# Kernel optimization log

Hardware: AMD Instinct MI355X
Metric: run time of the kernel (lower is better)

Reference implementation:

```python
import jax, jax.numpy as jnp
import numpy as np

HIDDEN = 2048
N_HEADS = 16
HEAD_DIM = 128
N_KV_HEADS = 4
MAX_POS = 4096
NEG_INF = -1e9


def _fixed_pos_embedding(features, length):
    # matches generate_fixed_pos_embedding: freqs over arange(0, features, 2)/features
    fraction = jnp.arange(0, features, 2, dtype=jnp.float32) / features
    timescale = 10000.0 ** fraction
    inv_freq = 1.0 / timescale
    sinusoid = jnp.einsum('i,j->ij', jnp.arange(length, dtype=jnp.float32), inv_freq)
    sinusoid = jnp.concatenate([sinusoid, sinusoid], axis=-1)  # [length, features]
    return jnp.sin(sinusoid), jnp.cos(sinusoid)


def setup_inputs() -> dict:
    key = jax.random.key(0)
    k0, k1, k2, k3, k4 = jax.random.split(key, 5)
    B, S = 2, 2048
    hidden_states = jax.random.normal(k0, (B, S, HIDDEN), dtype=jnp.float32)
    # causal additive mask [B,1,S,S]; module forces mask[:, :, :, 0] = 0
    causal = jnp.where(jnp.tril(jnp.ones((S, S), dtype=bool)), 0.0, NEG_INF).astype(jnp.float32)
    causal = causal.at[:, 0].set(0.0)
    attention_mask = jnp.broadcast_to(causal[None, None], (B, 1, S, S))
    std = 0.02
    q_w = jax.random.normal(k1, (N_HEADS * HEAD_DIM, HIDDEN), dtype=jnp.float32) * std
    k_w = jax.random.normal(k2, (N_KV_HEADS * HEAD_DIM, HIDDEN), dtype=jnp.float32) * std
    v_w = jax.random.normal(k3, (N_KV_HEADS * HEAD_DIM, HIDDEN), dtype=jnp.float32) * std
    o_w = jax.random.normal(k4, (HIDDEN, N_HEADS * HEAD_DIM), dtype=jnp.float32) * std
    sin, cos = _fixed_pos_embedding(HEAD_DIM, MAX_POS)
    return {"hidden_states": hidden_states, "attention_mask": attention_mask,
            "q_w": q_w, "k_w": k_w, "v_w": v_w, "o_w": o_w, "sin": sin, "cos": cos}


def _rotate_half(x):
    d = x.shape[-1] // 2
    return jnp.concatenate([-x[..., d:], x[..., :d]], axis=-1)


def reference(hidden_states, attention_mask, q_w, k_w, v_w, o_w, sin, cos):
    B, S, _ = hidden_states.shape
    D = cos.shape[-1]
    H = q_w.shape[0] // D
    KV = k_w.shape[0] // D
    n_rep = H // KV

    # QKV projections (nn.Linear: y = x @ W^T), split into heads: [B,S,h,D]
    q = jnp.einsum('bsh,oh->bso', hidden_states, q_w).reshape(B, S, H, D)
    k = jnp.einsum('bsh,oh->bso', hidden_states, k_w).reshape(B, S, KV, D)
    v = jnp.einsum('bsh,oh->bso', hidden_states, v_w).reshape(B, S, KV, D)

    # rotary embedding (non-decode path: q and k share cos/sin[:S])
    c = cos[:S][None, :, None, :]
    s = sin[:S][None, :, None, :]
    q = q * c + _rotate_half(q) * s
    k = k * c + _rotate_half(k) * s

    # repeat_kv (repeat_interleave along head dim) for GQA
    k = jnp.repeat(k, n_rep, axis=2)  # [B,S,H,D]
    v = jnp.repeat(v, n_rep, axis=2)

    # NOTE: no 1/sqrt(D) scaling -- module uses softmax_scale=1.0
    scores = jnp.einsum('bqhd,bkhd->bhqk', q, k) + attention_mask
    weights = jax.nn.softmax(scores.astype(jnp.float32), axis=-1).astype(q.dtype)
    attn = jnp.einsum('bhqk,bkhd->bqhd', weights, v).reshape(B, S, H * D)
    return jnp.einsum('bso,ho->bsh', attn, o_w)
```

## Files before the change

kernel.cpp:

```cpp
#include <hip/hip_runtime.h>

typedef __bf16 bf16x8 __attribute__((ext_vector_type(8)));
typedef float f32x4 __attribute__((ext_vector_type(4)));
typedef float f32x16 __attribute__((ext_vector_type(16)));

#define LOG2E 1.44269504088896340736f

#define GLDS16(g, l) __builtin_amdgcn_global_load_lds(                         \
    (const __attribute__((address_space(1))) unsigned int*)(g),                \
    (__attribute__((address_space(3))) unsigned int*)(l), 16, 0, 0)


__global__ __launch_bounds__(256) void megasplit(
    const float* __restrict__ hs, const float* __restrict__ qw,
    const float* __restrict__ kw, const float* __restrict__ vw,
    const float* __restrict__ ow,
    __bf16* __restrict__ hsh, __bf16* __restrict__ hsl,
    __bf16* __restrict__ wqh, __bf16* __restrict__ wql,
    __bf16* __restrict__ owh, __bf16* __restrict__ owl)
{
    int bid = blockIdx.x;
    const float* src; __bf16* dh; __bf16* dl;
    if (bid < 4096)      { src = hs; dh = hsh; dl = hsl; }
    else if (bid < 6144) { bid -= 4096; src = qw; dh = wqh; dl = wql; }
    else if (bid < 6656) { bid -= 6144; src = kw;
                           dh = wqh + (size_t)2048 * 2048;
                           dl = wql + (size_t)2048 * 2048; }
    else if (bid < 7168) { bid -= 6656; src = vw;
                           dh = wqh + (size_t)2560 * 2048;
                           dl = wql + (size_t)2560 * 2048; }
    else                 { bid -= 7168; src = ow; dh = owh; dl = owl; }

    const size_t t = (size_t)(bid * 256 + threadIdx.x) * 8;
    float4 a = *(const float4*)(src + t);
    float4 b = *(const float4*)(src + t + 4);
    float f[8] = {a.x, a.y, a.z, a.w, b.x, b.y, b.z, b.w};
    bf16x8 h, l;
#pragma unroll
    for (int i = 0; i < 8; ++i) {
        __bf16 hh = (__bf16)f[i];
        h[i] = hh; l[i] = (__bf16)(f[i] - (float)hh);
    }
    const int r  = (int)(t >> 11);
    const int sw = (r ^ (r >> 2)) & 3;
    const size_t d = (t & ~(size_t)31) + ((size_t)((((int)(t >> 3) & 3) ^ sw)) << 3);
    *(bf16x8*)(dh + d) = h;
    *(bf16x8*)(dl + d) = l;
}

template<int BN, int NLOAD>
__global__ __launch_bounds__(512, 2) void gemm_planes32(
    const __bf16* __restrict__ Ah, const __bf16* __restrict__ Al,
    const __bf16* __restrict__ Bh, const __bf16* __restrict__ Bl,
    float* __restrict__ C, int ldc)
{
    constexpr int WN = BN / 2;
    constexpr int CF = WN / 32;
    constexpr int RF = 2;

    __shared__ __bf16 sAh[2][256 * 32];
    __shared__ __bf16 sAl[2][256 * 32];
    __shared__ __bf16 sBh[2][BN * 32];
    __shared__ __bf16 sBl[2][BN * 32];

    const int tid  = threadIdx.x;
    const int lane = tid & 63;
    const int wave = tid >> 6;
    const int wmr  = (wave & 3) * 64;
    const int wnc  = (wave >> 2) * WN;

    const int idg = blockIdx.y * 16 + blockIdx.x;
    const int swb = (idg & 7) * 32 + (idg >> 3);
    const int m0  = (swb >> 4) * 256;
    const int n0  = (swb & 15) * BN;

    const int rl  = lane & 31;
    const int kh  = lane >> 5;
    const int srl = (rl ^ (rl >> 2)) & 3;

    const int srow = tid >> 2;
    const int spb  = (tid & 3) << 3;
    const __bf16* gAh0 = Ah + (size_t)(m0 + srow) * 2048 + spb;
    const __bf16* gAh1 = gAh0 + (size_t)128 * 2048;
    const __bf16* gAl0 = Al + (size_t)(m0 + srow) * 2048 + spb;
    const __bf16* gAl1 = gAl0 + (size_t)128 * 2048;
    const __bf16* gBh0 = Bh + (size_t)(n0 + srow) * 2048 + spb;
    const __bf16* gBl0 = Bl + (size_t)(n0 + srow) * 2048 + spb;
    const __bf16* gX5  = Bl;
    const __bf16* gBl6 = Bl;
    if constexpr (BN == 192) {
        gX5 = (tid < 256)
            ? Bh + (size_t)(n0 + 128 + srow) * 2048 + spb
            : Bl + (size_t)(n0 + ((tid - 256) >> 2)) * 2048 + (((tid - 256) & 3) << 3);
        gBl6 = Bl + (size_t)(n0 + 64 + srow) * 2048 + spb;
    }

#define STAGE8(bb)                                                             \
    do {                                                                       \
        GLDS16(gAh0, &sAh[bb][tid * 8]);                                       \
        GLDS16(gAh1, &sAh[bb][4096 + tid * 8]);                                \
        GLDS16(gAl0, &sAl[bb][tid * 8]);                                       \
        GLDS16(gAl1, &sAl[bb][4096 + tid * 8]);                                \
        GLDS16(gBh0, &sBh[bb][tid * 8]);                                       \
        if constexpr (BN == 192) {                                             \
            if (tid < 256) { GLDS16(gX5, &sBh[bb][4096 + tid * 8]); }          \
            else           { GLDS16(gX5, &sBl[bb][(tid - 256) * 8]); }         \
            GLDS16(gBl6, &sBl[bb][2048 + tid * 8]);                            \
        } else {                                                               \
            GLDS16(gBl0, &sBl[bb][tid * 8]);                                   \
        }                                                                      \
    } while (0)

#define ADV8()                                                                 \
    do {                                                                       \
        gAh0 += 32; gAh1 += 32; gAl0 += 32; gAl1 += 32;                        \
        gBh0 += 32; gBl0 += 32;                                                \
        if constexpr (BN == 192) { gX5 += 32; gBl6 += 32; }                    \
    } while (0)

    f32x16 acc[RF][CF];
#pragma unroll
    for (int rf = 0; rf < RF; ++rf)
#pragma unroll
        for (int cf = 0; cf < CF; ++cf)
            acc[rf][cf] = (f32x16){0.f};

    STAGE8(0);
    ADV8();

    for (int t = 0; t < 64; ++t) {
        const int buf = t & 1;

        __builtin_amdgcn_sched_barrier(0);
        asm volatile("s_waitcnt vmcnt(0)" ::: "memory");
        __builtin_amdgcn_sched_barrier(0);
        __builtin_amdgcn_s_barrier();
        __builtin_amdgcn_sched_barrier(0);
        if (t < 63) {
            STAGE8(buf ^ 1);
            ADV8();
        }
        __builtin_amdgcn_sched_barrier(0);

        __builtin_amdgcn_s_setprio(1);
#pragma unroll
        for (int kk = 0; kk < 2; ++kk) {
            bf16x8 ah[RF], al[RF], bhf[CF], blf[CF];
#pragma unroll
            for (int rf = 0; rf < RF; ++rf) {
                const int ra = (wmr + rf * 32 + rl) * 32
                             + (((kk * 2 + kh) ^ srl) << 3);
                ah[rf] = *(const bf16x8*)&sAh[buf][ra];
                al[rf] = *(const bf16x8*)&sAl[buf][ra];
            }
#pragma unroll
            for (int cf = 0; cf < CF; ++cf) {
                const int rb = (wnc + cf * 32 + rl) * 32
                             + (((kk * 2 + kh) ^ srl) << 3);
                bhf[cf] = *(const bf16x8*)&sBh[buf][rb];
                blf[cf] = *(const bf16x8*)&sBl[buf][rb];
            }
#pragma unroll
            for (int rf = 0; rf < RF; ++rf)
#pragma unroll
                for (int cf = 0; cf < CF; ++cf) {
                    acc[rf][cf] = __builtin_amdgcn_mfma_f32_32x32x16_bf16(
                        ah[rf], bhf[cf], acc[rf][cf], 0, 0, 0);
                    acc[rf][cf] = __builtin_amdgcn_mfma_f32_32x32x16_bf16(
                        al[rf], bhf[cf], acc[rf][cf], 0, 0, 0);
                    acc[rf][cf] = __builtin_amdgcn_mfma_f32_32x32x16_bf16(
                        ah[rf], blf[cf], acc[rf][cf], 0, 0, 0);
                }
        }
        __builtin_amdgcn_s_setprio(0);
    }

#pragma unroll
    for (int rf = 0; rf < RF; ++rf)
#pragma unroll
        for (int cf = 0; cf < CF; ++cf)
#pragma unroll
            for (int reg = 0; reg < 16; ++reg) {
                const int row = m0 + wmr + rf * 32
                              + (reg & 3) + 8 * (reg >> 2) + 4 * kh;
                const int col = n0 + wnc + cf * 32 + rl;
                C[(size_t)row * ldc + col] = acc[rf][cf][reg];
            }
#undef STAGE8
#undef ADV8
}

__global__ __launch_bounds__(256) void rope_prep(
    float* __restrict__ qkv,
    const float* __restrict__ sinp, const float* __restrict__ cosp,
    __bf16* __restrict__ ksp, __bf16* __restrict__ vtsp)
{
    __shared__ float vs[32][132];
    const int tid = threadIdx.x;

    if (blockIdx.x < 16384) {
        int t = blockIdx.x * 256 + tid;
        int row = t >> 10;
        int rem = t & 1023;
        int col = (rem >> 6) * 128 + (rem & 63);
        int s = row & 2047;
        int d = col & 127;

        float* p = qkv + (size_t)row * 3072 + col;
        float x0  = p[0];
        float x1  = p[64];
        float c0  = cosp[s * 128 + d];
        float c1  = cosp[s * 128 + d + 64];
        float sn0 = sinp[s * 128 + d];
        float sn1 = sinp[s * 128 + d + 64];
        p[0]  = x0 * c0 - x1 * sn0;
        p[64] = x1 * c1 + x0 * sn1;
        return;
    }

    const int pidx = blockIdx.x - 16384;
    const int kb  = pidx & 15;
    const int kvh = (pidx >> 4) & 3;
    const int b   = pidx >> 6;

    {
        const int key = tid >> 1;
        const int dh  = (tid & 1) * 32;
        const int pos = kb * 128 + key;
        const int ksw = key & 7;
        const float* src = qkv + (size_t)(b * 2048 + pos) * 3072 + 2048 + kvh * 128;
        __bf16* dst = ksp + ((size_t)((b * 4 + kvh) * 2048) + pos) * 256;
        const float* cp = cosp + pos * 128;
        const float* sp = sinp + pos * 128;
#pragma unroll
        for (int g = 0; g < 4; ++g) {
            int d0 = dh + g * 8;
            float4 x0a = *(const float4*)(src + d0);
            float4 x0b = *(const float4*)(src + d0 + 4);
            float4 x1a = *(const float4*)(src + d0 + 64);
            float4 x1b = *(const float4*)(src + d0 + 68);
            float4 c0a = *(const float4*)(cp + d0);
            float4 c0b = *(const float4*)(cp + d0 + 4);
            float4 c1a = *(const float4*)(cp + d0 + 64);
            float4 c1b = *(const float4*)(cp + d0 + 68);
            float4 s0a = *(const float4*)(sp + d0);
            float4 s0b = *(const float4*)(sp + d0 + 4);
            float4 s1a = *(const float4*)(sp + d0 + 64);
            float4 s1b = *(const float4*)(sp + d0 + 68);
            float x0[8] = {x0a.x,x0a.y,x0a.z,x0a.w,x0b.x,x0b.y,x0b.z,x0b.w};
            float x1[8] = {x1a.x,x1a.y,x1a.z,x1a.w,x1b.x,x1b.y,x1b.z,x1b.w};
            float c0[8] = {c0a.x,c0a.y,c0a.z,c0a.w,c0b.x,c0b.y,c0b.z,c0b.w};
            float c1[8] = {c1a.x,c1a.y,c1a.z,c1a.w,c1b.x,c1b.y,c1b.z,c1b.w};
            float s0[8] = {s0a.x,s0a.y,s0a.z,s0a.w,s0b.x,s0b.y,s0b.z,s0b.w};
            float s1[8] = {s1a.x,s1a.y,s1a.z,s1a.w,s1b.x,s1b.y,s1b.z,s1b.w};
            bf16x8 h0, l0, h1, l1;
#pragma unroll
            for (int i = 0; i < 8; ++i) {
                float y0 = x0[i] * c0[i] - x1[i] * s0[i];
                float y1 = x1[i] * c1[i] + x0[i] * s1[i];
                __bf16 hh0 = (__bf16)y0;
                __bf16 hh1 = (__bf16)y1;
                h0[i] = hh0; l0[i] = (__bf16)(y0 - (float)hh0);
                h1[i] = hh1; l1[i] = (__bf16)(y1 - (float)hh1);
            }
            const int bb = d0 >> 3;
            *(bf16x8*)(dst + ((bb        ^ ksw) << 3)) = h0;
            *(bf16x8*)(dst + (((bb + 8)  ^ ksw) << 3)) = h1;
            *(bf16x8*)(dst + (((bb + 16) ^ ksw) << 3)) = l0;
            *(bf16x8*)(dst + (((bb + 24) ^ ksw) << 3)) = l1;
        }
    }

    for (int st = 0; st < 4; ++st) {
        __syncthreads();
        {
            const int key = tid >> 3;
            const int dc  = (tid & 7) * 16;
            const float* vsrc = qkv + (size_t)(b * 2048 + kb * 128 + st * 32 + key) * 3072
                                + 2560 + kvh * 128 + dc;
            float4 v0 = *(const float4*)(vsrc);
            float4 v1 = *(const float4*)(vsrc + 4);
            float4 v2 = *(const float4*)(vsrc + 8);
            float4 v3 = *(const float4*)(vsrc + 12);
            *(float4*)&vs[key][dc]      = v0;
            *(float4*)&vs[key][dc + 4]  = v1;
            *(float4*)&vs[key][dc + 8]  = v2;
            *(float4*)&vs[key][dc + 12] = v3;
        }
        __syncthreads();
        {
            const int plane = tid >> 7;
            const int d     = tid & 127;
            bf16x8 ob[4];
#pragma unroll
            for (int k = 0; k < 32; ++k) {
                float x = vs[k][d];
                __bf16 hh = (__bf16)x;
                ob[k >> 3][k & 7] = plane ? (__bf16)(x - (float)hh) : hh;
            }
            const int rV  = plane * 128 + d;
            const int vsw = (d >> 1) & 3;
            __bf16* dst = vtsp + ((size_t)((b * 4 + kvh) * 64 + kb * 4 + st)) * 8192
                               + (size_t)rV * 32;
            *(bf16x8*)(dst + ((0 ^ vsw) << 3)) = ob[0];
            *(bf16x8*)(dst + ((1 ^ vsw) << 3)) = ob[1];
            *(bf16x8*)(dst + ((2 ^ vsw) << 3)) = ob[2];
            *(bf16x8*)(dst + ((3 ^ vsw) << 3)) = ob[3];
        }
    }
}

__global__ __launch_bounds__(512, 4) void flash_attn(
    const float* __restrict__ qkv,
    const __bf16* __restrict__ ksp,
    const __bf16* __restrict__ vtsp,
    __bf16* __restrict__ attnh, __bf16* __restrict__ attnl)
{
    __shared__ __bf16 Ks[2][32 * 256];
    __shared__ __bf16 Vt[2][256 * 32];
    __shared__ unsigned int Psf[4][2][512];

    const int tid  = threadIdx.x;
    const int lane = tid & 63;
    const int wave = tid >> 6;
    const int hw   = wave & 3;
    const int rs   = wave >> 2;
    const int id   = blockIdx.x;
    const int pair = id & 7;
    const int kvh  = pair & 3;
    const int b    = pair >> 2;
    const int u    = id >> 3;
    const int qb   = (u >> 5) ? (u & 31) : 63 - (u & 31);
    const int h    = kvh * 4 + hw;

    const int fr  = lane & 15;
    const int g   = lane >> 4;
    const int fc  = g * 8;
    const int dr  = g * 4;
    const int frs = fr & 7;

    bf16x8 aqh[4], aql[4];
    {
        const size_t qrow = (size_t)(b * 2048 + qb * 32 + rs * 16 + fr) * 3072 + h * 128;
#pragma unroll
        for (int ks = 0; ks < 4; ++ks) {
            float4 qv[2];
            qv[0] = *(const float4*)(qkv + qrow + ks * 32 + fc);
            qv[1] = *(const float4*)(qkv + qrow + ks * 32 + fc + 4);
            const float* qf = (const float*)qv;
            bf16x8 h8, l8;
#pragma unroll
            for (int i = 0; i < 8; ++i) {
                float x = qf[i];
                __bf16 hh = (__bf16)x;
                h8[i] = hh; l8[i] = (__bf16)(x - (float)hh);
            }
            aqh[ks] = h8; aql[ks] = l8;
        }
    }
    asm volatile("s_waitcnt vmcnt(0)" ::: "memory");
    __builtin_amdgcn_sched_barrier(0);

    bf16x8 ones;
#pragma unroll
    for (int i = 0; i < 8; ++i) ones[i] = (__bf16)1.0f;

    f32x4 o[8];
#pragma unroll
    for (int dg = 0; dg < 8; ++dg) o[dg] = (f32x4){0.f, 0.f, 0.f, 0.f};
    f32x4 ls = (f32x4){0.f, 0.f, 0.f, 0.f};

    const int ntiles = qb + 1;
    const __bf16* kg0 = ksp + (size_t)(b * 4 + kvh) * 2048 * 256 + wave * 1024 + lane * 8;
    const __bf16* vg0 = vtsp + (size_t)(b * 4 + kvh) * 64 * 8192 + wave * 1024 + lane * 8;

    {
        __bf16* kl = &Ks[0][wave * 1024];
        __bf16* vl = &Vt[0][wave * 1024];
        GLDS16(kg0, kl); GLDS16(kg0 + 512, kl + 512);
        GLDS16(vg0, vl); GLDS16(vg0 + 512, vl + 512);
    }

    for (int kt = 0; kt < ntiles; ++kt) {
        if (kt + 1 < ntiles) {
            const __bf16* kg = kg0 + (size_t)(kt + 1) * 8192;
            const __bf16* vg = vg0 + (size_t)(kt + 1) * 8192;
            __bf16* kl = &Ks[(kt + 1) & 1][wave * 1024];
            __bf16* vl = &Vt[(kt + 1) & 1][wave * 1024];
            GLDS16(kg, kl); GLDS16(kg + 512, kl + 512);
            GLDS16(vg, vl); GLDS16(vg + 512, vl + 512);
            asm volatile("s_waitcnt vmcnt(4)" ::: "memory");
        } else {
            asm volatile("s_waitcnt vmcnt(0)" ::: "memory");
        }
        __builtin_amdgcn_sched_barrier(0);
        __builtin_amdgcn_s_barrier();
        __builtin_amdgcn_sched_barrier(0);

        const int buf = kt & 1;
        const int k0 = kt * 32;

        f32x4 s0v = (f32x4){0.f, 0.f, 0.f, 0.f};
        f32x4 s1v = (f32x4){0.f, 0.f, 0.f, 0.f};
        __builtin_amdgcn_s_setprio(1);
#pragma unroll
        for (int ks = 0; ks < 4; ++ks) {
            const int bh = ks * 4 + g;
            bf16x8 b0h = *(const bf16x8*)&Ks[buf][fr * 256        + ((bh        ^ frs) << 3)];
            bf16x8 b0l = *(const bf16x8*)&Ks[buf][fr * 256        + (((bh + 16) ^ frs) << 3)];
            bf16x8 b1h = *(const bf16x8*)&Ks[buf][(16 + fr) * 256 + ((bh        ^ frs) << 3)];
            bf16x8 b1l = *(const bf16x8*)&Ks[buf][(16 + fr) * 256 + (((bh + 16) ^ frs) << 3)];
            s0v = __builtin_amdgcn_mfma_f32_16x16x32_bf16(aqh[ks], b0h, s0v, 0, 0, 0);
            s0v = __builtin_amdgcn_mfma_f32_16x16x32_bf16(aql[ks], b0h, s0v, 0, 0, 0);
            s0v = __builtin_amdgcn_mfma_f32_16x16x32_bf16(aqh[ks], b0l, s0v, 0, 0, 0);
            s1v = __builtin_amdgcn_mfma_f32_16x16x32_bf16(aqh[ks], b1h, s1v, 0, 0, 0);
            s1v = __builtin_amdgcn_mfma_f32_16x16x32_bf16(aql[ks], b1h, s1v, 0, 0, 0);
            s1v = __builtin_amdgcn_mfma_f32_16x16x32_bf16(aqh[ks], b1l, s1v, 0, 0, 0);
        }
        __builtin_amdgcn_s_setprio(0);

        if (kt == ntiles - 1) {
#pragma unroll
            for (int r = 0; r < 4; ++r) {
                const int qg = qb * 32 + rs * 16 + dr + r;
                if (k0 + fr > qg)      s0v[r] = -1e30f;
                if (k0 + 16 + fr > qg) s1v[r] = -1e30f;
            }
        }
        {
            uint4 w0, w1;
#pragma unroll
            for (int r = 0; r < 4; ++r) {
                float x0 = exp2f(s0v[r] * LOG2E);
                float x1 = exp2f(s1v[r] * LOG2E);
                __bf16 h0 = (__bf16)x0;
                __bf16 h1 = (__bf16)x1;
                unsigned u0 = ((unsigned)__builtin_bit_cast(unsigned short, h0) << 16)
                            |  (unsigned)__builtin_bit_cast(unsigned short, (__bf16)(x0 - (float)h0));
                unsigned u1 = ((unsigned)__builtin_bit_cast(unsigned short, h1) << 16)
                            |  (unsigned)__builtin_bit_cast(unsigned short, (__bf16)(x1 - (float)h1));
                ((unsigned*)&w0)[r] = u0;
                ((unsigned*)&w1)[r] = u1;
            }
            unsigned int* pw = &Psf[hw][rs][0];
            const int sb = (fr * 4 + g) ^ (((fr >> 3) & 1) << 2);
            *(uint4*)(pw + sb * 4)        = w0;
            *(uint4*)(pw + (sb + 64) * 4) = w1;
        }
        asm volatile("s_waitcnt lgkmcnt(0)" ::: "memory");
        __builtin_amdgcn_sched_barrier(0);

        bf16x8 ph, pl;
#pragma unroll
        for (int j = 0; j < 8; ++j) {
            const int col = fc + j;
            const int sR  = (col * 4 + (fr >> 2)) ^ ((g & 1) << 2);
            const unsigned v = Psf[hw][rs][sR * 4 + (fr & 3)];
            ph[j] = __builtin_bit_cast(__bf16, (unsigned short)(v >> 16));
            pl[j] = __builtin_bit_cast(__bf16, (unsigned short)(v & 0xffffu));
        }

        __builtin_amdgcn_s_setprio(1);
        ls = __builtin_amdgcn_mfma_f32_16x16x32_bf16(ph, ones, ls, 0, 0, 0);
        ls = __builtin_amdgcn_mfma_f32_16x16x32_bf16(pl, ones, ls, 0, 0, 0);
#pragma unroll
        for (int dg = 0; dg < 8; ++dg) {
            const int d0 = dg * 16 + fr;
            const int sw = (g ^ ((d0 >> 1) & 3)) << 3;
            bf16x8 bvh = *(const bf16x8*)&Vt[buf][d0 * 32 + sw];
            bf16x8 bvl = *(const bf16x8*)&Vt[buf][(d0 + 128) * 32 + sw];
            o[dg] = __builtin_amdgcn_mfma_f32_16x16x32_bf16(ph, bvh, o[dg], 0, 0, 0);
            o[dg] = __builtin_amdgcn_mfma_f32_16x16x32_bf16(pl, bvh, o[dg], 0, 0, 0);
            o[dg] = __builtin_amdgcn_mfma_f32_16x16x32_bf16(ph, bvl, o[dg], 0, 0, 0);
        }
        __builtin_amdgcn_s_setprio(0);

        __builtin_amdgcn_s_barrier();
    }

    {
        const size_t orow = (size_t)(b * 2048 + qb * 32 + rs * 16);
#pragma unroll
        for (int dg = 0; dg < 8; ++dg)
#pragma unroll
            for (int r = 0; r < 4; ++r) {
                float val = o[dg][r] / ls[r];
                const int rl  = dr + r;
                const int swz = (rl ^ (rl >> 2)) & 3;
                const int col = h * 128 + dg * 16 + fr;
                const size_t idx = (size_t)(orow + rl) * 2048 + (col & ~31)
                                 + ((((col >> 3) & 3) ^ swz) << 3) + (col & 7);
                __bf16 hh = (__bf16)val;
                attnh[idx] = hh;
                attnl[idx] = (__bf16)(val - (float)hh);
            }
    }
}

extern "C" void kernel_launch(void* const* d_in, const int* in_sizes, int n_in,
                              void* d_out, int out_size, void* d_ws, size_t ws_size,
                              hipStream_t stream)
{
    const float* hs   = (const float*)d_in[0];
    const float* qw   = (const float*)d_in[2];
    const float* kw   = (const float*)d_in[3];
    const float* vw   = (const float*)d_in[4];
    const float* ow   = (const float*)d_in[5];
    const float* sinp = (const float*)d_in[6];
    const float* cosp = (const float*)d_in[7];
    float* outp = (float*)d_out;

    char* w = (char*)d_ws;
    float*  qkv  = (float*)w;   w += (size_t)4096 * 3072 * 4;
    __bf16* ksp  = (__bf16*)w;  w += (size_t)8 * 2048 * 256 * 2;
    __bf16* vtsp = (__bf16*)w;  w += (size_t)8 * 64 * 8192 * 2;
    __bf16* wqh  = (__bf16*)w;  w += (size_t)3072 * 2048 * 2;
    __bf16* wql  = (__bf16*)w;  w += (size_t)3072 * 2048 * 2;
    __bf16* owh  = (__bf16*)w;  w += (size_t)2048 * 2048 * 2;
    __bf16* owl  = (__bf16*)w;  w += (size_t)2048 * 2048 * 2;
    __bf16* hsh  = (__bf16*)w;  w += (size_t)4096 * 2048 * 2;
    __bf16* hsl  = (__bf16*)w;  w += (size_t)4096 * 2048 * 2;
    __bf16* attnh = hsh;
    __bf16* attnl = hsl;

    megasplit<<<9216, 256, 0, stream>>>(hs, qw, kw, vw, ow,
                                        hsh, hsl, wqh, wql, owh, owl);
    gemm_planes32<192, 7><<<dim3(16, 16), 512, 0, stream>>>(hsh, hsl, wqh, wql, qkv, 3072);
    rope_prep<<<16512, 256, 0, stream>>>(qkv, sinp, cosp, ksp, vtsp);
    flash_attn<<<512, 512, 0, stream>>>(qkv, ksp, vtsp, attnh, attnl);
    gemm_planes32<128, 6><<<dim3(16, 16), 512, 0, stream>>>(attnh, attnl, owh, owl, outp, 2048);
}
```

Baseline: 570.8 us.

## Pair complementary causal q-blocks within a workgroup and reswizzle P scratch

Each workgroup's two wave groups now process 16-row halves of mirrored query blocks (u and 63-u) instead of two halves of the same block, sharing one K/V tile stream. The group with the shorter causal range skips compute once past its diagonal but keeps hitting barriers. The intent is to balance causal work across workgroups and share K/V loads. The P staging buffer is also made per-wave with a new XOR swizzle to reduce LDS bank conflicts. The risk is idle waves stalling at barriers and longer-lived workgroups.

```diff
diff --git a/kernel.cpp b/kernel.cpp
--- a/kernel.cpp
+++ b/kernel.cpp
@@ -318,19 +318,22 @@
 {
     __shared__ __bf16 Ks[2][32 * 256];
     __shared__ __bf16 Vt[2][256 * 32];
-    __shared__ unsigned int Psf[4][2][512];
+    __shared__ unsigned int Psf[8][512];
 
     const int tid  = threadIdx.x;
     const int lane = tid & 63;
     const int wave = tid >> 6;
     const int hw   = wave & 3;
-    const int rs   = wave >> 2;
+    const int sel  = wave >> 2;
     const int id   = blockIdx.x;
     const int pair = id & 7;
     const int kvh  = pair & 3;
     const int b    = pair >> 2;
-    const int u    = id >> 3;
-    const int qb   = (u >> 5) ? (u & 31) : 63 - (u & 31);
+    const int v    = id >> 3;
+    const int u    = v & 31;
+    const int h2   = v >> 5;
+    const int qbw  = sel ? (63 - u) : u;
+    const int qbase= qbw * 32 + h2 * 16;
     const int h    = kvh * 4 + hw;
 
     const int fr  = lane & 15;
@@ -341,7 +344,7 @@
 
     bf16x8 aqh[4], aql[4];
     {
-        const size_t qrow = (size_t)(b * 2048 + qb * 32 + rs * 16 + fr) * 3072 + h * 128;
+        const size_t qrow = (size_t)(b * 2048 + qbase + fr) * 3072 + h * 128;
 #pragma unroll
         for (int ks = 0; ks < 4; ++ks) {
             float4 qv[2];
@@ -370,7 +373,7 @@
     for (int dg = 0; dg < 8; ++dg) o[dg] = (f32x4){0.f, 0.f, 0.f, 0.f};
     f32x4 ls = (f32x4){0.f, 0.f, 0.f, 0.f};
 
-    const int ntiles = qb + 1;
+    const int ntiles = 64 - u;
     const __bf16* kg0 = ksp + (size_t)(b * 4 + kvh) * 2048 * 256 + wave * 1024 + lane * 8;
     const __bf16* vg0 = vtsp + (size_t)(b * 4 + kvh) * 64 * 8192 + wave * 1024 + lane * 8;
 
@@ -400,86 +403,92 @@
         const int buf = kt & 1;
         const int k0 = kt * 32;
 
-        f32x4 s0v = (f32x4){0.f, 0.f, 0.f, 0.f};
-        f32x4 s1v = (f32x4){0.f, 0.f, 0.f, 0.f};
-        __builtin_amdgcn_s_setprio(1);
-#pragma unroll
-        for (int ks = 0; ks < 4; ++ks) {
-            const int bh = ks * 4 + g;
-            bf16x8 b0h = *(const bf16x8*)&Ks[buf][fr * 256        + ((bh        ^ frs) << 3)];
-            bf16x8 b0l = *(const bf16x8*)&Ks[buf][fr * 256        + (((bh + 16) ^ frs) << 3)];
-            bf16x8 b1h = *(const bf16x8*)&Ks[buf][(16 + fr) * 256 + ((bh        ^ frs) << 3)];
-            bf16x8 b1l = *(const bf16x8*)&Ks[buf][(16 + fr) * 256 + (((bh + 16) ^ frs) << 3)];
-            s0v = __builtin_amdgcn_mfma_f32_16x16x32_bf16(aqh[ks], b0h, s0v, 0, 0, 0);
-            s0v = __builtin_amdgcn_mfma_f32_16x16x32_bf16(aql[ks], b0h, s0v, 0, 0, 0);
-            s0v = __builtin_amdgcn_mfma_f32_16x16x32_bf16(aqh[ks], b0l, s0v, 0, 0, 0);
-            s1v = __builtin_amdgcn_mfma_f32_16x16x32_bf16(aqh[ks], b1h, s1v, 0, 0, 0);
-            s1v = __builtin_amdgcn_mfma_f32_16x16x32_bf16(aql[ks], b1h, s1v, 0, 0, 0);
-            s1v = __builtin_amdgcn_mfma_f32_16x16x32_bf16(aqh[ks], b1l, s1v, 0, 0, 0);
-        }
-        __builtin_amdgcn_s_setprio(0);
-
-        if (kt == ntiles - 1) {
-#pragma unroll
-            for (int r = 0; r < 4; ++r) {
-                const int qg = qb * 32 + rs * 16 + dr + r;
-                if (k0 + fr > qg)      s0v[r] = -1e30f;
-                if (k0 + 16 + fr > qg) s1v[r] = -1e30f;
-            }
-        }
-        {
-            uint4 w0, w1;
-#pragma unroll
-            for (int r = 0; r < 4; ++r) {
-                float x0 = exp2f(s0v[r] * LOG2E);
-                float x1 = exp2f(s1v[r] * LOG2E);
-                __bf16 h0 = (__bf16)x0;
-                __bf16 h1 = (__bf16)x1;
-                unsigned u0 = ((unsigned)__builtin_bit_cast(unsigned short, h0) << 16)
-                            |  (unsigned)__builtin_bit_cast(unsigned short, (__bf16)(x0 - (float)h0));
-                unsigned u1 = ((unsigned)__builtin_bit_cast(unsigned short, h1) << 16)
-                            |  (unsigned)__builtin_bit_cast(unsigned short, (__bf16)(x1 - (float)h1));
-                ((unsigned*)&w0)[r] = u0;
-                ((unsigned*)&w1)[r] = u1;
-            }
-            unsigned int* pw = &Psf[hw][rs][0];
-            const int sb = (fr * 4 + g) ^ (((fr >> 3) & 1) << 2);
-            *(uint4*)(pw + sb * 4)        = w0;
-            *(uint4*)(pw + (sb + 64) * 4) = w1;
-        }
-        asm volatile("s_waitcnt lgkmcnt(0)" ::: "memory");
-        __builtin_amdgcn_sched_barrier(0);
-
-        bf16x8 ph, pl;
-#pragma unroll
-        for (int j = 0; j < 8; ++j) {
-            const int col = fc + j;
-            const int sR  = (col * 4 + (fr >> 2)) ^ ((g & 1) << 2);
-            const unsigned v = Psf[hw][rs][sR * 4 + (fr & 3)];
-            ph[j] = __builtin_bit_cast(__bf16, (unsigned short)(v >> 16));
-            pl[j] = __builtin_bit_cast(__bf16, (unsigned short)(v & 0xffffu));
-        }
-
-        __builtin_amdgcn_s_setprio(1);
-        ls = __builtin_amdgcn_mfma_f32_16x16x32_bf16(ph, ones, ls, 0, 0, 0);
-        ls = __builtin_amdgcn_mfma_f32_16x16x32_bf16(pl, ones, ls, 0, 0, 0);
-#pragma unroll
-        for (int dg = 0; dg < 8; ++dg) {
-            const int d0 = dg * 16 + fr;
-            const int sw = (g ^ ((d0 >> 1) & 3)) << 3;
-            bf16x8 bvh = *(const bf16x8*)&Vt[buf][d0 * 32 + sw];
-            bf16x8 bvl = *(const bf16x8*)&Vt[buf][(d0 + 128) * 32 + sw];
-            o[dg] = __builtin_amdgcn_mfma_f32_16x16x32_bf16(ph, bvh, o[dg], 0, 0, 0);
-            o[dg] = __builtin_amdgcn_mfma_f32_16x16x32_bf16(pl, bvh, o[dg], 0, 0, 0);
-            o[dg] = __builtin_amdgcn_mfma_f32_16x16x32_bf16(ph, bvl, o[dg], 0, 0, 0);
-        }
-        __builtin_amdgcn_s_setprio(0);
+        if (kt <= qbw) {
+            f32x4 s0v = (f32x4){0.f, 0.f, 0.f, 0.f};
+            f32x4 s1v = (f32x4){0.f, 0.f, 0.f, 0.f};
+            __builtin_amdgcn_s_setprio(1);
+#pragma unroll
+            for (int ks = 0; ks < 4; ++ks) {
+                const int bh = ks * 4 + g;
+                bf16x8 b0h = *(const bf16x8*)&Ks[buf][fr * 256        + ((bh        ^ frs) << 3)];
+                bf16x8 b0l = *(const bf16x8*)&Ks[buf][fr * 256        + (((bh + 16) ^ frs) << 3)];
+                bf16x8 b1h = *(const bf16x8*)&Ks[buf][(16 + fr) * 256 + ((bh        ^ frs) << 3)];
+                bf16x8 b1l = *(const bf16x8*)&Ks[buf][(16 + fr) * 256 + (((bh + 16) ^ frs) << 3)];
+                s0v = __builtin_amdgcn_mfma_f32_16x16x32_bf16(aqh[ks], b0h, s0v, 0, 0, 0);
+                s0v = __builtin_amdgcn_mfma_f32_16x16x32_bf16(aql[ks], b0h, s0v, 0, 0, 0);
+                s0v = __builtin_amdgcn_mfma_f32_16x16x32_bf16(aqh[ks], b0l, s0v, 0, 0, 0);
+                s1v = __builtin_amdgcn_mfma_f32_16x16x32_bf16(aqh[ks], b1h, s1v, 0, 0, 0);
+                s1v = __builtin_amdgcn_mfma_f32_16x16x32_bf16(aql[ks], b1h, s1v, 0, 0, 0);
+                s1v = __builtin_amdgcn_mfma_f32_16x16x32_bf16(aqh[ks], b1l, s1v, 0, 0, 0);
+            }
+            __builtin_amdgcn_s_setprio(0);
+
+            if (kt == qbw) {
+#pragma unroll
+                for (int r = 0; r < 4; ++r) {
+                    const int qg = qbase + dr + r;
+                    if (k0 + fr > qg)      s0v[r] = -1e30f;
+                    if (k0 + 16 + fr > qg) s1v[r] = -1e30f;
+                }
+            }
+            {
+                uint4 w0, w1;
+#pragma unroll
+                for (int r = 0; r < 4; ++r) {
+                    float x0 = exp2f(s0v[r] * LOG2E);
+                    float x1 = exp2f(s1v[r] * LOG2E);
+                    __bf16 h0 = (__bf16)x0;
+                    __bf16 h1 = (__bf16)x1;
+                    unsigned u0 = ((unsigned)__builtin_bit_cast(unsigned short, h0) << 16)
+                                |  (unsigned)__builtin_bit_cast(unsigned short, (__bf16)(x0 - (float)h0));
+                    unsigned u1 = ((unsigned)__builtin_bit_cast(unsigned short, h1) << 16)
+                                |  (unsigned)__builtin_bit_cast(unsigned short, (__bf16)(x1 - (float)h1));
+                    ((unsigned*)&w0)[r] = u0;
+                    ((unsigned*)&w1)[r] = u1;
+                }
+                unsigned int* pw = &Psf[wave][0];
+                const int lg0 = fr * 4 + g;
+                const int lg1 = 64 + lg0;
+                const int sb0 = lg0 ^ ((lg0 >> 3) & 7);
+                const int sb1 = lg1 ^ ((lg1 >> 3) & 7);
+                *(uint4*)(pw + sb0 * 4) = w0;
+                *(uint4*)(pw + sb1 * 4) = w1;
+            }
+            asm volatile("s_waitcnt lgkmcnt(0)" ::: "memory");
+            __builtin_amdgcn_sched_barrier(0);
+
+            bf16x8 ph, pl;
+#pragma unroll
+            for (int j = 0; j < 8; ++j) {
+                const int col = fc + j;
+                const int lgr = col * 4 + (fr >> 2);
+                const int sbr = lgr ^ ((lgr >> 3) & 7);
+                const unsigned pv = Psf[wave][sbr * 4 + (fr & 3)];
+                ph[j] = __builtin_bit_cast(__bf16, (unsigned short)(pv >> 16));
+                pl[j] = __builtin_bit_cast(__bf16, (unsigned short)(pv & 0xffffu));
+            }
+
+            __builtin_amdgcn_s_setprio(1);
+            ls = __builtin_amdgcn_mfma_f32_16x16x32_bf16(ph, ones, ls, 0, 0, 0);
+            ls = __builtin_amdgcn_mfma_f32_16x16x32_bf16(pl, ones, ls, 0, 0, 0);
+#pragma unroll
+            for (int dg = 0; dg < 8; ++dg) {
+                const int d0 = dg * 16 + fr;
+                const int sw = (g ^ ((d0 >> 1) & 3)) << 3;
+                bf16x8 bvh = *(const bf16x8*)&Vt[buf][d0 * 32 + sw];
+                bf16x8 bvl = *(const bf16x8*)&Vt[buf][(d0 + 128) * 32 + sw];
+                o[dg] = __builtin_amdgcn_mfma_f32_16x16x32_bf16(ph, bvh, o[dg], 0, 0, 0);
+                o[dg] = __builtin_amdgcn_mfma_f32_16x16x32_bf16(pl, bvh, o[dg], 0, 0, 0);
+                o[dg] = __builtin_amdgcn_mfma_f32_16x16x32_bf16(ph, bvl, o[dg], 0, 0, 0);
+            }
+            __builtin_amdgcn_s_setprio(0);
+        }
 
         __builtin_amdgcn_s_barrier();
     }
 
     {
-        const size_t orow = (size_t)(b * 2048 + qb * 32 + rs * 16);
+        const size_t orow = (size_t)(b * 2048 + qbase);
 #pragma unroll
         for (int dg = 0; dg < 8; ++dg)
 #pragma unroll
```

Result: slower. 614.8 us (+7.7%).
